# Performance work log

Measured on AMD Instinct MI355X. Metric: run time of the kernel, lower is better.

Reference implementation:

```python
import jax, jax.numpy as jnp
import numpy as np

B, S, D, H, FF = 2, 2048, 512, 8, 2048
DK = D // H
EPS = 1e-5


def layer_norm(x, g, b):
    mu = jnp.mean(x, axis=-1, keepdims=True)
    var = jnp.mean((x - mu) ** 2, axis=-1, keepdims=True)
    return (x - mu) / jnp.sqrt(var + EPS) * g + b


def split_heads(x):  # [B,S,D] -> [B,H,S,DK]
    b, s, _ = x.shape
    return x.reshape(b, s, H, DK).transpose(0, 2, 1, 3)


def merge_heads(x):  # [B,H,S,DK] -> [B,S,D]
    b, h, s, dk = x.shape
    return x.transpose(0, 2, 1, 3).reshape(b, s, h * dk)


def mha(q_in, kv, in_w, in_b, out_w, out_b):
    # torch nn.MultiheadAttention, batch_first, eval mode (no dropout)
    Wq, Wk, Wv = in_w[:D], in_w[D:2 * D], in_w[2 * D:]
    bq, bk, bv = in_b[:D], in_b[D:2 * D], in_b[2 * D:]
    q = split_heads(q_in @ Wq.T + bq)
    k = split_heads(kv @ Wk.T + bk)
    v = split_heads(kv @ Wv.T + bv)
    scores = jnp.einsum('bhqd,bhkd->bhqk', q, k) / jnp.sqrt(jnp.float32(DK))
    attn = jax.nn.softmax(scores, axis=-1)
    out = merge_heads(jnp.einsum('bhqk,bhkd->bhqd', attn, v))
    return out @ out_w.T + out_b


def setup_inputs() -> dict:
    key = jax.random.key(0)
    ks = jax.random.split(key, 32)
    p = lambda k, shape: (jax.random.normal(k, shape, jnp.float32) * 0.02)
    inp = {
        'x_q': jax.random.normal(ks[0], (B, S, D), jnp.float32),
        'x1': jax.random.normal(ks[1], (B, S, D), jnp.float32),
        'x2': jax.random.normal(ks[2], (B, S, D), jnp.float32),
        # causal self-attention projections (no output proj in original)
        'sa_wq': p(ks[3], (D, D)), 'sa_bq': jnp.zeros((D,), jnp.float32),
        'sa_wk': p(ks[4], (D, D)), 'sa_bk': jnp.zeros((D,), jnp.float32),
        'sa_wv': p(ks[5], (D, D)), 'sa_bv': jnp.zeros((D,), jnp.float32),
        'ln1_g': jnp.ones((D,), jnp.float32), 'ln1_b': jnp.zeros((D,), jnp.float32),
        # shared cross-attention (cross_attn used twice in forward)
        'mha_in_w': p(ks[6], (3 * D, D)), 'mha_in_b': jnp.zeros((3 * D,), jnp.float32),
        'mha_out_w': p(ks[7], (D, D)), 'mha_out_b': jnp.zeros((D,), jnp.float32),
        # shared add_norm2 (used twice)
        'ln2_g': jnp.ones((D,), jnp.float32), 'ln2_b': jnp.zeros((D,), jnp.float32),
        # FFN
        'ffn_w1': p(ks[8], (FF, D)), 'ffn_b1': jnp.zeros((FF,), jnp.float32),
        'ffn_w2': p(ks[9], (D, FF)), 'ffn_b2': jnp.zeros((D,), jnp.float32),
        # add_norm3 (final)
        'ln3_g': jnp.ones((D,), jnp.float32), 'ln3_b': jnp.zeros((D,), jnp.float32),
    }
    return inp


def reference(x_q, x1, x2, sa_wq, sa_bq, sa_wk, sa_bk, sa_wv, sa_bv,
              ln1_g, ln1_b, mha_in_w, mha_in_b, mha_out_w, mha_out_b,
              ln2_g, ln2_b, ffn_w1, ffn_b1, ffn_w2, ffn_b2, ln3_g, ln3_b):
    # --- causal self-attention (hand-rolled, masked_fill with -1e9) ---
    q = split_heads(x_q @ sa_wq.T + sa_bq)
    k = split_heads(x_q @ sa_wk.T + sa_bk)
    v = split_heads(x_q @ sa_wv.T + sa_bv)
    scores = jnp.einsum('bhqd,bhkd->bhqk', q, k) / jnp.sqrt(jnp.float32(DK))
    causal = jnp.tril(jnp.ones((S, S), dtype=bool))
    scores = jnp.where(causal[None, None], scores, jnp.float32(-1e9))
    attn = jax.nn.softmax(scores, axis=-1)
    y_sa = merge_heads(jnp.einsum('bhqk,bhkd->bhqd', attn, v))
    y = layer_norm(x_q + y_sa, ln1_g, ln1_b)
    # --- cross-attention 1 (shared weights) + shared add_norm2 ---
    yattn = mha(y, x1, mha_in_w, mha_in_b, mha_out_w, mha_out_b)
    yattn = layer_norm(y + yattn, ln2_g, ln2_b)
    # --- cross-attention 2 (SAME module/weights as cross-attn 1) ---
    yattn2 = mha(yattn, x2, mha_in_w, mha_in_b, mha_out_w, mha_out_b)
    yattn2 = layer_norm(yattn + yattn2, ln2_g, ln2_b)
    # --- FFN + add_norm3 ---
    h = jax.nn.relu(yattn2 @ ffn_w1.T + ffn_b1)
    ff = h @ ffn_w2.T + ffn_b2
    return layer_norm(yattn2 + ff, ln3_g, ln3_b)
```

## Files before the change

kernel.cpp:

```cpp
#include <hip/hip_runtime.h>
#include <hip/hip_bf16.h>

#define S_LEN 2048
#define DMODEL 512
#define NHEAD 8
#define DKH 64
#define FFDIM 2048
#define BATCH 2
#define NROWS (BATCH * S_LEN)

using bf16 = __hip_bfloat16;
typedef __bf16 bf16x8 __attribute__((ext_vector_type(8)));
typedef float floatx4 __attribute__((ext_vector_type(4)));
typedef float floatx16 __attribute__((ext_vector_type(16)));

__device__ inline unsigned short f2bf_bits(float f) {
    union { float f; unsigned u; } c; c.f = f;
    return (unsigned short)((c.u + 0x7FFFu + ((c.u >> 16) & 1u)) >> 16);
}
__device__ inline unsigned pack2bf(float a, float b) {
    return (unsigned)f2bf_bits(a) | ((unsigned)f2bf_bits(b) << 16);
}
__device__ inline unsigned pk2(float a, float b) {
    float2 f; f.x = a; f.y = b;
    __hip_bfloat162 h = __float22bfloat162_rn(f);
    return *(unsigned*)&h;
}

__device__ __forceinline__ void gload_lds16(const bf16* g, bf16* l) {
    __builtin_amdgcn_global_load_lds(
        (const __attribute__((address_space(1))) void*)(const void*)g,
        (__attribute__((address_space(3))) void*)(void*)l, 16, 0, 0);
}

struct CvtSeg { const float* s; bf16* d; int n4; };
struct CvtDesc { CvtSeg seg[12]; };

__launch_bounds__(256)
__global__ void cvt_f32_bf16(CvtDesc desc) {
    const CvtSeg sg = desc.seg[blockIdx.y];
    const int stride = gridDim.x * 256;
    for (int i = blockIdx.x * 256 + threadIdx.x; i < sg.n4; i += stride) {
        const float4 v = ((const float4*)sg.s)[i];
        uint2 o;
        o.x = pack2bf(v.x, v.y);
        o.y = pack2bf(v.z, v.w);
        ((uint2*)sg.d)[i] = o;
    }
}

struct Epi {
    bf16*  outB[3];
    float* outF[3];
    const float* bias[3];
    float scale[3];
    const bf16* A2;
    int a2slab;
    int shift;
    int relu;
};

template <int BM, int BN>
__launch_bounds__(256)
__global__ void gemm2(const bf16* __restrict__ A, const bf16* __restrict__ W,
                      Epi epi, int K)
{
    constexpr int WR = BM / 32;
    constexpr int WC = BN / 32;
    constexpr int SA = BM / 16;
    constexpr int SB = BN / 16;
    constexpr int NG = 2 * (SA + SB);

    __shared__ alignas(16) bf16 As[2][BM][32];
    __shared__ alignas(16) bf16 Bs[2][BN][32];

    const int t = threadIdx.x;
    const int w = t >> 6;
    const int lane = t & 63;
    const int r16 = lane & 15;
    const int quad = lane >> 4;
    const int wm = w >> 1, wn = w & 1;
    const int m0 = blockIdx.x * BM;
    const int n0 = blockIdx.y * BN;

    const bf16* Ause = (epi.A2 && ((n0 >> epi.shift) >= epi.a2slab)) ? epi.A2 : A;

    floatx4 acc[WR][WC];
#pragma unroll
    for (int i = 0; i < WR; i++)
#pragma unroll
        for (int j = 0; j < WC; j++)
#pragma unroll
            for (int e = 0; e < 4; e++) acc[i][j][e] = 0.0f;

    const int grow = lane >> 2;
    const int gcol = (lane & 3) * 8;

    for (int k0 = 0; k0 < K; k0 += 64) {
        __syncthreads();
#pragma unroll
        for (int s = 0; s < NG; s += 4) {
            int sg = s + w;
            int p = 0;
            if (sg >= SA + SB) { p = 1; sg -= SA + SB; }
            const bf16* src;
            bf16* dst;
            if (sg < SA) {
                src = Ause + (size_t)(m0 + sg * 16 + grow) * K + k0 + 32 * p + gcol;
                dst = &As[p][sg * 16][0] + lane * 8;
            } else {
                const int sb = sg - SA;
                src = W + (size_t)(n0 + sb * 16 + grow) * K + k0 + 32 * p + gcol;
                dst = &Bs[p][sb * 16][0] + lane * 8;
            }
            gload_lds16(src, dst);
        }
        __syncthreads();

        bf16x8 af[2][WR], bfr[2][WC];
#pragma unroll
        for (int p = 0; p < 2; p++) {
#pragma unroll
            for (int i = 0; i < WR; i++)
                af[p][i] = *(const bf16x8*)&As[p][wm * (BM / 2) + 16 * i + r16][quad * 8];
#pragma unroll
            for (int j = 0; j < WC; j++)
                bfr[p][j] = *(const bf16x8*)&Bs[p][wn * (BN / 2) + 16 * j + r16][quad * 8];
        }
#pragma unroll
        for (int p = 0; p < 2; p++)
#pragma unroll
            for (int i = 0; i < WR; i++)
#pragma unroll
                for (int j = 0; j < WC; j++)
                    acc[i][j] = __builtin_amdgcn_mfma_f32_16x16x32_bf16(af[p][i], bfr[p][j], acc[i][j], 0, 0, 0);
    }

    const int mask = (1 << epi.shift) - 1;
#pragma unroll
    for (int j = 0; j < WC; j++) {
        const int colb = n0 + wn * (BN / 2) + 16 * j;
        const int sel = __builtin_amdgcn_readfirstlane(colb >> epi.shift);
        const int lcol = (colb & mask) + r16;
        const int ldw = mask + 1;
        const float bv = epi.bias[sel] ? epi.bias[sel][lcol] : 0.0f;
        const float sc = epi.scale[sel];
        bf16* ob = epi.outB[sel];
        float* of = epi.outF[sel];
#pragma unroll
        for (int i = 0; i < WR; i++) {
            const int rowb = m0 + wm * (BM / 2) + 16 * i + 4 * quad;
#pragma unroll
            for (int e = 0; e < 4; e++) {
                float v = (acc[i][j][e] + bv) * sc;
                if (epi.relu) v = fmaxf(v, 0.0f);
                const size_t idx = (size_t)(rowb + e) * ldw + lcol;
                if (of) of[idx] = v;
                if (ob) ob[idx] = __float2bfloat16(v);
            }
        }
    }
}

#define KST 72
#define PST2 44

__launch_bounds__(512, 2)
__global__ void attn_mfma(const bf16* __restrict__ Qh, const bf16* __restrict__ Kh,
                          const bf16* __restrict__ Vh,
                          float* __restrict__ outF, bf16* __restrict__ outB,
                          int causal)
{
    __shared__ alignas(16) char smem[40960];
    typedef bf16 (*KsT)[KST];
    KsT Ks = (KsT)smem;
    KsT Vt = (KsT)(smem + 9216);
    typedef bf16 (*PsT)[32][PST2];
    PsT Ps = (PsT)(smem + 18432);
    typedef float (*MshT)[64][34];
    MshT Msh = (MshT)smem;

    const int t = threadIdx.x;
    const int w = t >> 6;
    const int lane = t & 63;
    const int c32 = lane & 31;
    const int hi = lane >> 5;
    const int qg = w >> 1;
    const int kh = w & 1;
    const int bh = blockIdx.y;
    const int b = bh >> 3, h = bh & 7;
    const int q0 = blockIdx.x * 128;
    const size_t rowbase = (size_t)b * S_LEN;
    const int hoff = h * DKH;

    bf16x8 qf[4];
    {
        const bf16* qp = Qh + (rowbase + q0 + qg * 32 + c32) * DMODEL + hoff + 8 * hi;
#pragma unroll
        for (int tt = 0; tt < 4; tt++) qf[tt] = *(const bf16x8*)(qp + 16 * tt);
    }

    floatx16 o0, o1;
#pragma unroll
    for (int e = 0; e < 16; e++) { o0[e] = 0.0f; o1[e] = 0.0f; }
    float m = -3e38f, l = 0.0f;

    const int krow = t >> 3;
    const int kcol = (t & 7) * 8;
    const int pl = t - 256;
    const int rq = pl & 15;
    const int c8 = ((pl >> 4) & 7) * 8;

    const int nchunk = causal ? (q0 / 64 + 2) : (S_LEN / 64);

    for (int ch = 0; ch < nchunk; ch++) {
        const int kb = ch * 64;
        __syncthreads();

        if (t < 256) {
            const bf16* kp = Kh + (rowbase + kb + krow) * DMODEL + hoff + kcol;
            uint4 ka = *(const uint4*)(kp);
            uint4 kc = *(const uint4*)(kp + (size_t)32 * DMODEL);
            *(uint4*)&Ks[krow][kcol] = ka;
            *(uint4*)&Ks[krow + 32][kcol] = kc;
        } else if (t < 384) {
            union { uint4 u; unsigned short s[8]; } r0, r1, r2, r3;
            const bf16* vb = Vh + (rowbase + kb + 4 * rq) * DMODEL + hoff + c8;
            r0.u = *(const uint4*)(vb);
            r1.u = *(const uint4*)(vb + DMODEL);
            r2.u = *(const uint4*)(vb + 2 * DMODEL);
            r3.u = *(const uint4*)(vb + 3 * DMODEL);
#pragma unroll
            for (int j = 0; j < 8; j++) {
                ushort4 pk = { r0.s[j], r1.s[j], r2.s[j], r3.s[j] };
                *(ushort4*)&Vt[c8 + j][4 * rq] = pk;
            }
        }

        __syncthreads();

        bf16x8 kf[4];
#pragma unroll
        for (int tt = 0; tt < 4; tt++)
            kf[tt] = *(const bf16x8*)&Ks[kh * 32 + c32][16 * tt + 8 * hi];

        floatx16 s;
#pragma unroll
        for (int e = 0; e < 16; e++) s[e] = 0.0f;
        __builtin_amdgcn_s_setprio(1);
#pragma unroll
        for (int tt = 0; tt < 4; tt++)
            s = __builtin_amdgcn_mfma_f32_32x32x16_bf16(kf[tt], qf[tt], s, 0, 0, 0);
        __builtin_amdgcn_s_setprio(0);

        if (causal && ch >= nchunk - 2) {
            const int qq = q0 + qg * 32 + c32;
#pragma unroll
            for (int r = 0; r < 16; r++) {
                const int kl = kb + kh * 32 + (r & 3) + 8 * (r >> 2) + 4 * hi;
                if (kl > qq) s[r] = -3e38f;
            }
        }

        float mc = -3e38f;
#pragma unroll
        for (int r = 0; r < 16; r++) mc = fmaxf(mc, s[r]);
        mc = fmaxf(mc, __shfl_xor(mc, 32, 64));

        float alpha = 1.0f;
        if (!__all(mc <= m + 8.0f)) {
            const float mold = m;
            m = fmaxf(m, mc);
            alpha = __builtin_amdgcn_exp2f(mold - m);
#pragma unroll
            for (int r = 0; r < 16; r++) {
                const float a = __shfl(alpha, (r & 3) + 8 * (r >> 2) + 4 * hi, 64);
                o0[r] *= a; o1[r] *= a;
            }
        }

        float lc = 0.0f;
#pragma unroll
        for (int g = 0; g < 4; g++) {
            float p0 = __builtin_amdgcn_exp2f(s[4 * g + 0] - m);
            float p1 = __builtin_amdgcn_exp2f(s[4 * g + 1] - m);
            float p2 = __builtin_amdgcn_exp2f(s[4 * g + 2] - m);
            float p3 = __builtin_amdgcn_exp2f(s[4 * g + 3] - m);
            lc += (p0 + p1) + (p2 + p3);
            uint2 pw; pw.x = pk2(p0, p1); pw.y = pk2(p2, p3);
            *(uint2*)&Ps[w][c32][8 * g + 4 * hi] = pw;
        }
        lc += __shfl_xor(lc, 32, 64);
        l = l * alpha + lc;

        __builtin_amdgcn_s_setprio(1);
#pragma unroll
        for (int tt = 0; tt < 2; tt++) {
            const bf16x8 pf = *(const bf16x8*)&Ps[w][c32][16 * tt + 8 * hi];
            const bf16x8 v0 = *(const bf16x8*)&Vt[c32][kh * 32 + 16 * tt + 8 * hi];
            const bf16x8 v1 = *(const bf16x8*)&Vt[32 + c32][kh * 32 + 16 * tt + 8 * hi];
            o0 = __builtin_amdgcn_mfma_f32_32x32x16_bf16(pf, v0, o0, 0, 0, 0);
            o1 = __builtin_amdgcn_mfma_f32_32x32x16_bf16(pf, v1, o1, 0, 0, 0);
        }
        __builtin_amdgcn_s_setprio(0);
    }

    __syncthreads();
    if (kh == 1) {
        float* dst = &Msh[qg][lane][0];
        dst[0] = m; dst[1] = l;
#pragma unroll
        for (int r = 0; r < 16; r++) { dst[2 + r] = o0[r]; dst[18 + r] = o1[r]; }
    }
    __syncthreads();
    if (kh == 0) {
        const float* src = &Msh[qg][lane][0];
        const float m_b = src[0], l_b = src[1];
        const float mt = fmaxf(m, m_b);
        const float sA = __builtin_amdgcn_exp2f(m - mt);
        const float sB = __builtin_amdgcn_exp2f(m_b - mt);
        const float lt = l * sA + l_b * sB;
#pragma unroll
        for (int r = 0; r < 16; r++) {
            const int ql = (r & 3) + 8 * (r >> 2) + 4 * hi;
            const float sAr = __shfl(sA, ql, 64);
            const float sBr = __shfl(sB, ql, 64);
            const float li = 1.0f / __shfl(lt, ql, 64);
            const float v0 = (o0[r] * sAr + src[2 + r] * sBr) * li;
            const float v1 = (o1[r] * sAr + src[18 + r] * sBr) * li;
            const size_t idx = (rowbase + q0 + qg * 32 + ql) * DMODEL + hoff + c32;
            if (outF) { outF[idx] = v0; outF[idx + 32] = v1; }
            if (outB) { outB[idx] = __float2bfloat16(v0); outB[idx + 32] = __float2bfloat16(v1); }
        }
    }
}

__launch_bounds__(256)
__global__ void ln_kernel(const float* __restrict__ xmain,
                          const float* __restrict__ resF, const bf16* __restrict__ resB,
                          const float* __restrict__ g, const float* __restrict__ bb,
                          float* __restrict__ outF, bf16* __restrict__ outB)
{
    const int row = blockIdx.x;
    const int t = threadIdx.x;
    const size_t base = (size_t)row * DMODEL;

    float x0 = xmain[base + t];
    float x1 = xmain[base + t + 256];
    if (resF) { x0 += resF[base + t]; x1 += resF[base + t + 256]; }
    if (resB) { x0 += __bfloat162float(resB[base + t]); x1 += __bfloat162float(resB[base + t + 256]); }

    __shared__ float sred[4];
    float s = x0 + x1;
#pragma unroll
    for (int off = 32; off > 0; off >>= 1) s += __shfl_down(s, off);
    if ((t & 63) == 0) sred[t >> 6] = s;
    __syncthreads();
    const float mu = (sred[0] + sred[1] + sred[2] + sred[3]) * (1.0f / DMODEL);

    const float d0 = x0 - mu, d1 = x1 - mu;
    float sv = d0 * d0 + d1 * d1;
#pragma unroll
    for (int off = 32; off > 0; off >>= 1) sv += __shfl_down(sv, off);
    __syncthreads();
    if ((t & 63) == 0) sred[t >> 6] = sv;
    __syncthreads();
    const float var = (sred[0] + sred[1] + sred[2] + sred[3]) * (1.0f / DMODEL);
    const float rstd = rsqrtf(var + 1e-5f);

    const float y0 = d0 * rstd * g[t] + bb[t];
    const float y1 = d1 * rstd * g[t + 256] + bb[t + 256];
    if (outF) { outF[base + t] = y0; outF[base + t + 256] = y1; }
    if (outB) { outB[base + t] = __float2bfloat16(y0); outB[base + t + 256] = __float2bfloat16(y1); }
}

extern "C" void kernel_launch(void* const* d_in, const int* in_sizes, int n_in,
                              void* d_out, int out_size, void* d_ws, size_t ws_size,
                              hipStream_t stream)
{
    const float* x_q       = (const float*)d_in[0];
    const float* x1        = (const float*)d_in[1];
    const float* x2        = (const float*)d_in[2];
    const float* sa_wq     = (const float*)d_in[3];
    const float* sa_bq     = (const float*)d_in[4];
    const float* sa_wk     = (const float*)d_in[5];
    const float* sa_bk     = (const float*)d_in[6];
    const float* sa_wv     = (const float*)d_in[7];
    const float* sa_bv     = (const float*)d_in[8];
    const float* ln1_g     = (const float*)d_in[9];
    const float* ln1_b     = (const float*)d_in[10];
    const float* mha_in_w  = (const float*)d_in[11];
    const float* mha_in_b  = (const float*)d_in[12];
    const float* mha_out_w = (const float*)d_in[13];
    const float* mha_out_b = (const float*)d_in[14];
    const float* ln2_g     = (const float*)d_in[15];
    const float* ln2_b     = (const float*)d_in[16];
    const float* ffn_w1    = (const float*)d_in[17];
    const float* ffn_b1    = (const float*)d_in[18];
    const float* ffn_w2    = (const float*)d_in[19];
    const float* ffn_b2    = (const float*)d_in[20];
    const float* ln3_g     = (const float*)d_in[21];
    const float* ln3_b     = (const float*)d_in[22];

    char* ws = (char*)d_ws;
    const size_t MB = 1024 * 1024;
    const size_t KB = 1024;
    bf16*  q16  = (bf16*)(ws + 0 * MB);
    bf16*  k16  = (bf16*)(ws + 4 * MB);
    bf16*  v16  = (bf16*)(ws + 8 * MB);
    bf16*  a16  = (bf16*)(ws + 12 * MB);
    float* tmp  = (float*)(ws + 16 * MB);
    bf16*  y16  = (bf16*)(ws + 24 * MB);
    bf16*  ya16 = (bf16*)(ws + 28 * MB);
    bf16*  ya2  = (bf16*)(ws + 32 * MB);
    bf16*  xq16 = (bf16*)(ws + 36 * MB);
    bf16*  x116 = (bf16*)(ws + 40 * MB);
    bf16*  x216 = (bf16*)(ws + 44 * MB);
    bf16*  w_sa_qkv = (bf16*)(ws + 48 * MB);
    bf16*  w_in   = (bf16*)(ws + 49 * MB + 512 * KB);
    bf16*  w_out  = (bf16*)(ws + 51 * MB);
    bf16*  w_f1   = (bf16*)(ws + 51 * MB + 512 * KB);
    bf16*  w_f2   = (bf16*)(ws + 53 * MB + 512 * KB);
    bf16*  h16    = (bf16*)(ws + 0 * MB);

    const int DD = DMODEL * DMODEL;
    CvtDesc cd;
    cd.seg[0]  = { x_q,       xq16,        (NROWS * DMODEL) / 4 };
    cd.seg[1]  = { x1,        x116,        (NROWS * DMODEL) / 4 };
    cd.seg[2]  = { x2,        x216,        (NROWS * DMODEL) / 4 };
    cd.seg[3]  = { sa_wq,     w_sa_qkv,           DD / 4 };
    cd.seg[4]  = { sa_wk,     w_sa_qkv + DD,      DD / 4 };
    cd.seg[5]  = { sa_wv,     w_sa_qkv + 2 * DD,  DD / 4 };
    cd.seg[6]  = { mha_in_w,  w_in,   3 * DD / 4 };
    cd.seg[7]  = { mha_out_w, w_out,  DD / 4 };
    cd.seg[8]  = { ffn_w1,    w_f1,   (FFDIM * DMODEL) / 4 };
    cd.seg[9]  = { ffn_w2,    w_f2,   (FFDIM * DMODEL) / 4 };
    cd.seg[10] = { x_q,       xq16,   0 };
    cd.seg[11] = { x_q,       xq16,   0 };
    cvt_f32_bf16<<<dim3(64, 10), 256, 0, stream>>>(cd);

    const dim3 blk(256);
    const dim3 ablk(512);
    const dim3 agrid(S_LEN / 128, BATCH * NHEAD);

    const float QSC = 0.125f * 1.44269504088896f;

    Epi eQKV = {};
    eQKV.outB[0] = q16; eQKV.outB[1] = k16; eQKV.outB[2] = v16;
    eQKV.bias[0] = sa_bq; eQKV.bias[1] = sa_bk; eQKV.bias[2] = sa_bv;
    eQKV.scale[0] = QSC; eQKV.scale[1] = 1.0f; eQKV.scale[2] = 1.0f;
    eQKV.shift = 9;

    Epi eX1 = {};
    eX1.outB[0] = q16; eX1.outB[1] = k16; eX1.outB[2] = v16;
    eX1.bias[0] = mha_in_b; eX1.bias[1] = mha_in_b + DMODEL; eX1.bias[2] = mha_in_b + 2 * DMODEL;
    eX1.scale[0] = QSC; eX1.scale[1] = 1.0f; eX1.scale[2] = 1.0f;
    eX1.A2 = x116; eX1.a2slab = 1; eX1.shift = 9;

    Epi eX2 = eX1;
    eX2.A2 = x216;

    Epi eOut = {};
    eOut.outF[0] = tmp; eOut.bias[0] = mha_out_b; eOut.scale[0] = 1.0f; eOut.shift = 9;

    Epi eF1 = {};
    eF1.outB[0] = h16; eF1.bias[0] = ffn_b1; eF1.scale[0] = 1.0f;
    eF1.shift = 11; eF1.relu = 1;

    Epi eF2 = {};
    eF2.outF[0] = tmp; eF2.bias[0] = ffn_b2; eF2.scale[0] = 1.0f; eF2.shift = 9;

    gemm2<64, 64><<<dim3(64, 24), blk, 0, stream>>>(xq16, w_sa_qkv, eQKV, DMODEL);
    attn_mfma<<<agrid, ablk, 0, stream>>>(q16, k16, v16, tmp, nullptr, 1);
    ln_kernel<<<NROWS, blk, 0, stream>>>(tmp, x_q, nullptr, ln1_g, ln1_b, nullptr, y16);

    gemm2<64, 64><<<dim3(64, 24), blk, 0, stream>>>(y16, w_in, eX1, DMODEL);
    attn_mfma<<<agrid, ablk, 0, stream>>>(q16, k16, v16, nullptr, a16, 0);
    gemm2<64, 64><<<dim3(64, 8), blk, 0, stream>>>(a16, w_out, eOut, DMODEL);
    ln_kernel<<<NROWS, blk, 0, stream>>>(tmp, nullptr, y16, ln2_g, ln2_b, nullptr, ya16);

    gemm2<64, 64><<<dim3(64, 24), blk, 0, stream>>>(ya16, w_in, eX2, DMODEL);
    attn_mfma<<<agrid, ablk, 0, stream>>>(q16, k16, v16, nullptr, a16, 0);
    gemm2<64, 64><<<dim3(64, 8), blk, 0, stream>>>(a16, w_out, eOut, DMODEL);
    ln_kernel<<<NROWS, blk, 0, stream>>>(tmp, nullptr, ya16, ln2_g, ln2_b, nullptr, ya2);

    gemm2<128, 128><<<dim3(32, 16), blk, 0, stream>>>(ya2, w_f1, eF1, DMODEL);
    gemm2<64, 64><<<dim3(64, 8), blk, 0, stream>>>(h16, w_f2, eF2, FFDIM);
    ln_kernel<<<NROWS, blk, 0, stream>>>(tmp, nullptr, ya2, ln3_g, ln3_b, (float*)d_out, nullptr);
}
```

Before: 443.1 us.

## Halve attention query tile and double-buffer K/V with register prefetch

The attention kernel now uses 256-thread blocks covering 64 query rows instead of 512 threads covering 128, doubling the grid. The causal chunk count and diagonal masking are adjusted to match. K and V tiles move to double-buffered shared memory, with the next chunk's global loads prefetched into registers while the current one is computed. This cuts the loop to one barrier per chunk and hides load latency. It raises shared memory per block and register pressure, and each K/V tile is now loaded by twice as many blocks.

```diff
diff --git a/kernel.cpp b/kernel.cpp
--- a/kernel.cpp
+++ b/kernel.cpp
@@ -165,18 +165,18 @@
 #define KST 72
 #define PST2 44
 
-__launch_bounds__(512, 2)
+__launch_bounds__(256, 2)
 __global__ void attn_mfma(const bf16* __restrict__ Qh, const bf16* __restrict__ Kh,
                           const bf16* __restrict__ Vh,
                           float* __restrict__ outF, bf16* __restrict__ outB,
                           int causal)
 {
-    __shared__ alignas(16) char smem[40960];
-    typedef bf16 (*KsT)[KST];
-    KsT Ks = (KsT)smem;
-    KsT Vt = (KsT)(smem + 9216);
+    __shared__ alignas(16) char smem[48128];
+    typedef bf16 (*KbufT)[64][KST];
+    KbufT Ks = (KbufT)smem;
+    KbufT Vt = (KbufT)(smem + 18432);
     typedef bf16 (*PsT)[32][PST2];
-    PsT Ps = (PsT)(smem + 18432);
+    PsT Ps = (PsT)(smem + 36864);
     typedef float (*MshT)[64][34];
     MshT Msh = (MshT)smem;
 
@@ -189,7 +189,7 @@
     const int kh = w & 1;
     const int bh = blockIdx.y;
     const int b = bh >> 3, h = bh & 7;
-    const int q0 = blockIdx.x * 128;
+    const int q0 = blockIdx.x * 64;
     const size_t rowbase = (size_t)b * S_LEN;
     const int hoff = h * DKH;
 
@@ -207,42 +207,63 @@
 
     const int krow = t >> 3;
     const int kcol = (t & 7) * 8;
-    const int pl = t - 256;
+    const int pl = t & 127;
     const int rq = pl & 15;
     const int c8 = ((pl >> 4) & 7) * 8;
-
-    const int nchunk = causal ? (q0 / 64 + 2) : (S_LEN / 64);
+    const bool vstager = (t >= 128);
+
+    const int nchunk = causal ? (q0 / 64 + 1) : (S_LEN / 64);
+
+    uint4 kra, krb, vr0, vr1, vr2, vr3;
+    {
+        const bf16* kp = Kh + (rowbase + krow) * DMODEL + hoff + kcol;
+        kra = *(const uint4*)(kp);
+        krb = *(const uint4*)(kp + (size_t)32 * DMODEL);
+        if (vstager) {
+            const bf16* vb = Vh + (rowbase + 4 * rq) * DMODEL + hoff + c8;
+            vr0 = *(const uint4*)(vb);
+            vr1 = *(const uint4*)(vb + DMODEL);
+            vr2 = *(const uint4*)(vb + 2 * DMODEL);
+            vr3 = *(const uint4*)(vb + 3 * DMODEL);
+        }
+    }
 
     for (int ch = 0; ch < nchunk; ch++) {
+        const int buf = ch & 1;
         const int kb = ch * 64;
-        __syncthreads();
-
-        if (t < 256) {
-            const bf16* kp = Kh + (rowbase + kb + krow) * DMODEL + hoff + kcol;
-            uint4 ka = *(const uint4*)(kp);
-            uint4 kc = *(const uint4*)(kp + (size_t)32 * DMODEL);
-            *(uint4*)&Ks[krow][kcol] = ka;
-            *(uint4*)&Ks[krow + 32][kcol] = kc;
-        } else if (t < 384) {
+
+        *(uint4*)&Ks[buf][krow][kcol] = kra;
+        *(uint4*)&Ks[buf][krow + 32][kcol] = krb;
+        if (vstager) {
             union { uint4 u; unsigned short s[8]; } r0, r1, r2, r3;
-            const bf16* vb = Vh + (rowbase + kb + 4 * rq) * DMODEL + hoff + c8;
-            r0.u = *(const uint4*)(vb);
-            r1.u = *(const uint4*)(vb + DMODEL);
-            r2.u = *(const uint4*)(vb + 2 * DMODEL);
-            r3.u = *(const uint4*)(vb + 3 * DMODEL);
+            r0.u = vr0; r1.u = vr1; r2.u = vr2; r3.u = vr3;
 #pragma unroll
             for (int j = 0; j < 8; j++) {
                 ushort4 pk = { r0.s[j], r1.s[j], r2.s[j], r3.s[j] };
-                *(ushort4*)&Vt[c8 + j][4 * rq] = pk;
+                *(ushort4*)&Vt[buf][c8 + j][4 * rq] = pk;
             }
         }
 
+        if (ch + 1 < nchunk) {
+            const int kb1 = (ch + 1) * 64;
+            const bf16* kp = Kh + (rowbase + kb1 + krow) * DMODEL + hoff + kcol;
+            kra = *(const uint4*)(kp);
+            krb = *(const uint4*)(kp + (size_t)32 * DMODEL);
+            if (vstager) {
+                const bf16* vb = Vh + (rowbase + kb1 + 4 * rq) * DMODEL + hoff + c8;
+                vr0 = *(const uint4*)(vb);
+                vr1 = *(const uint4*)(vb + DMODEL);
+                vr2 = *(const uint4*)(vb + 2 * DMODEL);
+                vr3 = *(const uint4*)(vb + 3 * DMODEL);
+            }
+        }
+
         __syncthreads();
 
         bf16x8 kf[4];
 #pragma unroll
         for (int tt = 0; tt < 4; tt++)
-            kf[tt] = *(const bf16x8*)&Ks[kh * 32 + c32][16 * tt + 8 * hi];
+            kf[tt] = *(const bf16x8*)&Ks[buf][kh * 32 + c32][16 * tt + 8 * hi];
 
         floatx16 s;
 #pragma unroll
@@ -253,7 +274,7 @@
             s = __builtin_amdgcn_mfma_f32_32x32x16_bf16(kf[tt], qf[tt], s, 0, 0, 0);
         __builtin_amdgcn_s_setprio(0);
 
-        if (causal && ch >= nchunk - 2) {
+        if (causal && ch == nchunk - 1) {
             const int qq = q0 + qg * 32 + c32;
 #pragma unroll
             for (int r = 0; r < 16; r++) {
@@ -297,8 +318,8 @@
 #pragma unroll
         for (int tt = 0; tt < 2; tt++) {
             const bf16x8 pf = *(const bf16x8*)&Ps[w][c32][16 * tt + 8 * hi];
-            const bf16x8 v0 = *(const bf16x8*)&Vt[c32][kh * 32 + 16 * tt + 8 * hi];
-            const bf16x8 v1 = *(const bf16x8*)&Vt[32 + c32][kh * 32 + 16 * tt + 8 * hi];
+            const bf16x8 v0 = *(const bf16x8*)&Vt[buf][c32][kh * 32 + 16 * tt + 8 * hi];
+            const bf16x8 v1 = *(const bf16x8*)&Vt[buf][32 + c32][kh * 32 + 16 * tt + 8 * hi];
             o0 = __builtin_amdgcn_mfma_f32_32x32x16_bf16(pf, v0, o0, 0, 0, 0);
             o1 = __builtin_amdgcn_mfma_f32_32x32x16_bf16(pf, v1, o1, 0, 0, 0);
         }
@@ -440,8 +461,8 @@
     cvt_f32_bf16<<<dim3(64, 10), 256, 0, stream>>>(cd);
 
     const dim3 blk(256);
-    const dim3 ablk(512);
-    const dim3 agrid(S_LEN / 128, BATCH * NHEAD);
+    const dim3 ablk(256);
+    const dim3 agrid(S_LEN / 64, BATCH * NHEAD);
 
     const float QSC = 0.125f * 1.44269504088896f;
 
```

Result: faster. 409.6 us (-7.6%).
